# Optimization experiments

Hardware: AMD Instinct MI355X
Metric: run time of the kernel (lower is better)

Reference implementation:

```python
import jax, jax.numpy as jnp
import numpy as np

DIM = 768
HEADS = 12
HEAD_DIM = DIM // HEADS
SCALE = HEAD_DIM ** -0.5


def setup_inputs() -> dict:
    key = jax.random.key(0)
    k1, k2, k3, k4 = jax.random.split(key, 4)
    x = jax.random.normal(k1, (1, 4096, DIM), dtype=jnp.float32)
    # qkv: Linear(dim, 3*dim), bias=False
    W_qkv = jax.random.normal(k2, (DIM, 3 * DIM), dtype=jnp.float32) * (DIM ** -0.5)
    # proj: Linear(dim, dim) with bias
    W_proj = jax.random.normal(k3, (DIM, DIM), dtype=jnp.float32) * (DIM ** -0.5)
    b_proj = jax.random.normal(k4, (DIM,), dtype=jnp.float32) * 0.01
    return {"x": x, "W_qkv": W_qkv, "W_proj": W_proj, "b_proj": b_proj}


def reference(x, W_qkv, W_proj, b_proj):
    b, n, d = x.shape
    qkv = x @ W_qkv                                  # [b, n, 3d]
    q, k, v = jnp.split(qkv, 3, axis=-1)             # each [b, n, d]
    # split heads: [b, n, (h hd)] -> [b, h, n, hd]
    def heads(t):
        return t.reshape(b, n, HEADS, HEAD_DIM).transpose(0, 2, 1, 3)
    q, k, v = heads(q) * SCALE, heads(k), heads(v)
    sim = jnp.einsum('bhid,bhjd->bhij', q, k)        # [b, h, n, n] -- full score matrix
    attn = jax.nn.softmax(sim, axis=-1)
    out = jnp.einsum('bhij,bhjd->bhid', attn, v)     # [b, h, n, hd]
    out = out.transpose(0, 2, 1, 3).reshape(b, n, d)  # merge heads
    return out @ W_proj + b_proj
```

## Files before the change

### kernel.cpp

```cpp
#include <hip/hip_runtime.h>
#include <math.h>

#define TOKENS 4096
#define DMODEL 768
#define NHEADS 12
#define HDIM   64
#define QKV_N  2304
#define ATTN_SCALE 0.125f
#define QSCALE_LOG2E (0.125f * 1.44269504088896340736f)

typedef __attribute__((ext_vector_type(8))) short bf16x8;
typedef __attribute__((ext_vector_type(4))) float floatx4;

__device__ __forceinline__ ushort f2bf(float f) {
    union { float f; unsigned u; } cv; cv.f = f;
    unsigned u = cv.u;
    u += 0x7fffu + ((u >> 16) & 1u);
    return (ushort)(u >> 16);
}

__device__ __forceinline__ unsigned pack_bf16_rne(float a, float b) {
    union { float f; unsigned u; } ca, cb; ca.f = a; cb.f = b;
    unsigned ua = ca.u + 0x7fffu + ((ca.u >> 16) & 1u);
    unsigned ub = cb.u + 0x7fffu + ((cb.u >> 16) & 1u);
    return __builtin_amdgcn_perm(ub, ua, 0x07060302);
}

__device__ __forceinline__ void gl2lds16(const ushort* g, ushort* l) {
    __builtin_amdgcn_global_load_lds(
        (const __attribute__((address_space(1))) void*)g,
        (__attribute__((address_space(3))) void*)l, 16, 0, 0);
}

__device__ __forceinline__ bf16x8 frag(const ushort* ls, int row, int chunk) {
    return *(const bf16x8*)(ls + row * 64 + ((chunk ^ (row & 7)) * 8));
}

__global__ __launch_bounds__(256) void cvt_bf16_kernel(
    const float* __restrict__ in, ushort* __restrict__ out, int n4)
{
    const int i = blockIdx.x * 256 + threadIdx.x;
    if (i < n4) {
        const float4 v = ((const float4*)in)[i];
        ushort4 h;
        h.x = f2bf(v.x); h.y = f2bf(v.y); h.z = f2bf(v.z); h.w = f2bf(v.w);
        ((ushort4*)out)[i] = h;
    }
}

__global__ __launch_bounds__(256) void transpose_cvt_kernel(
    const float* __restrict__ in, ushort* __restrict__ out, int R, int C)
{
    __shared__ ushort tile[32][33];
    const int tx  = threadIdx.x & 31;
    const int ty8 = threadIdx.x >> 5;
    const int c0 = blockIdx.x * 32;
    const int r0 = blockIdx.y * 32;
    #pragma unroll
    for (int p = 0; p < 4; ++p) {
        const int r = ty8 + p * 8;
        tile[r][tx] = f2bf(in[(size_t)(r0 + r) * C + c0 + tx]);
    }
    __syncthreads();
    #pragma unroll
    for (int p = 0; p < 4; ++p) {
        const int c = ty8 + p * 8;
        out[(size_t)(c0 + c) * R + r0 + tx] = tile[tx][c];
    }
}

template<int NT>
__device__ __forceinline__ void gemm_body_async(
    const ushort* __restrict__ A, const ushort* __restrict__ Bt, int K,
    int m0, int n0, floatx4 acc[4][NT], ushort* ls)
{
    ushort* lsA = ls;
    ushort* lsB = ls + 8192;

    const int tid  = threadIdx.x;
    const int lane = tid & 63;
    const int wave = tid >> 6;
    const int wm = wave >> 1, wn = wave & 1;
    const int quad = lane >> 4, l16 = lane & 15;

    const int lrow = lane >> 3;
    const int csw  = ((lane & 7) ^ lrow) * 8;

    const ushort* gA = A  + (size_t)(m0 + wave * 32 + lrow) * K + csw;
    const ushort* gB = Bt + (size_t)(n0 + wave * NT * 8 + lrow) * K + csw;
    ushort* lA = lsA + (wave * 32) * 64;
    ushort* lB = lsB + (wave * NT * 8) * 64;

    for (int k0 = 0; k0 < K; k0 += 64) {
        __syncthreads();
        #pragma unroll
        for (int p = 0; p < 4; ++p)
            gl2lds16(gA + (size_t)p * 8 * K + k0, lA + p * 8 * 64);
        #pragma unroll
        for (int p = 0; p < NT; ++p)
            gl2lds16(gB + (size_t)p * 8 * K + k0, lB + p * 8 * 64);
        __syncthreads();

        #pragma unroll
        for (int ks = 0; ks < 2; ++ks) {
            bf16x8 af[4], bfr[NT];
            #pragma unroll
            for (int mt = 0; mt < 4; ++mt)
                af[mt] = frag(lsA, wm * 64 + mt * 16 + l16, ks * 4 + quad);
            #pragma unroll
            for (int nt = 0; nt < NT; ++nt)
                bfr[nt] = frag(lsB, wn * NT * 16 + nt * 16 + l16, ks * 4 + quad);
            #pragma unroll
            for (int mt = 0; mt < 4; ++mt)
                #pragma unroll
                for (int nt = 0; nt < NT; ++nt)
                    acc[mt][nt] = __builtin_amdgcn_mfma_f32_16x16x32_bf16(
                        af[mt], bfr[nt], acc[mt][nt], 0, 0, 0);
        }
    }
}

__global__ __launch_bounds__(256) void gemm_qkv_mfma(
    const ushort* __restrict__ Xb, const ushort* __restrict__ Wt,
    ushort* __restrict__ Qb, ushort* __restrict__ Kb, ushort* __restrict__ Vt)
{
    __shared__ __align__(16) ushort ls[16384];
    const int m0 = blockIdx.y * 128;
    const int n0 = blockIdx.x * 128;

    floatx4 acc[4][4] = {};
    gemm_body_async<4>(Xb, Wt, DMODEL, m0, n0, acc, ls);

    const int tid  = threadIdx.x;
    const int lane = tid & 63;
    const int wave = tid >> 6;
    const int wm = wave >> 1, wn = wave & 1;
    const int quad = lane >> 4, l16 = lane & 15;

    if (n0 < 2 * DMODEL) {
        const float scale = (n0 < DMODEL) ? QSCALE_LOG2E : 1.0f;
        ushort* outp = (n0 < DMODEL) ? Qb : Kb;
        const int colg = (n0 < DMODEL) ? n0 : n0 - DMODEL;
        #pragma unroll
        for (int p = 0; p < 2; ++p) {
            __syncthreads();
            if (wm == p) {
                #pragma unroll
                for (int mt = 0; mt < 4; ++mt)
                    #pragma unroll
                    for (int nt = 0; nt < 4; ++nt) {
                        const int row = mt * 16 + quad * 4;
                        const int col = wn * 64 + nt * 16 + l16;
                        #pragma unroll
                        for (int r = 0; r < 4; ++r)
                            ls[(row + r) * 136 + col] = f2bf(acc[mt][nt][r] * scale);
                    }
            }
            __syncthreads();
            #pragma unroll
            for (int p2 = 0; p2 < 4; ++p2) {
                const int row = (tid >> 4) + p2 * 16;
                const int c8  = (tid & 15) * 8;
                *(uint4*)(outp + (size_t)(m0 + p * 64 + row) * DMODEL + colg + c8) =
                    *(const uint4*)(ls + row * 136 + c8);
            }
        }
    } else {
        const int hd0 = n0 - 2 * DMODEL;
        #pragma unroll
        for (int p = 0; p < 2; ++p) {
            __syncthreads();
            if (wn == p) {
                #pragma unroll
                for (int mt = 0; mt < 4; ++mt)
                    #pragma unroll
                    for (int nt = 0; nt < 4; ++nt) {
                        const int hd  = nt * 16 + l16;
                        const int tok = wm * 64 + mt * 16 + quad * 4;
                        #pragma unroll
                        for (int r = 0; r < 4; ++r)
                            ls[hd * 136 + tok + r] = f2bf(acc[mt][nt][r]);
                    }
            }
            __syncthreads();
            #pragma unroll
            for (int p2 = 0; p2 < 4; ++p2) {
                const int row = (tid >> 4) + p2 * 16;
                const int c8  = (tid & 15) * 8;
                *(uint4*)(Vt + (size_t)(hd0 + p * 64 + row) * TOKENS + m0 + c8) =
                    *(const uint4*)(ls + row * 136 + c8);
            }
        }
    }
}

__global__ __launch_bounds__(256) void gemm_proj_mfma(
    const ushort* __restrict__ Ab, const ushort* __restrict__ Wt,
    const float* __restrict__ bias, float* __restrict__ out)
{
    __shared__ __align__(16) ushort ls[12288];
    const int m0 = blockIdx.y * 128;
    const int n0 = blockIdx.x * 64;

    floatx4 acc[4][2] = {};
    gemm_body_async<2>(Ab, Wt, DMODEL, m0, n0, acc, ls);

    const int lane = threadIdx.x & 63;
    const int wave = threadIdx.x >> 6;
    const int wm = wave >> 1, wn = wave & 1;
    const int quad = lane >> 4, l16 = lane & 15;
    const int row0 = m0 + wm * 64 + quad * 4;
    const int col0 = n0 + wn * 32;

    #pragma unroll
    for (int nt = 0; nt < 2; ++nt) {
        const int col = col0 + nt * 16 + l16;
        const float bv = bias[col];
        #pragma unroll
        for (int mt = 0; mt < 4; ++mt)
            #pragma unroll
            for (int r = 0; r < 4; ++r)
                out[(size_t)(row0 + mt * 16 + r) * DMODEL + col] =
                    acc[mt][nt][r] + bv;
    }
}

__global__ __launch_bounds__(256) void attn_mfma_kernel(
    const ushort* __restrict__ Qb, const ushort* __restrict__ Kb,
    const ushort* __restrict__ Vt, ushort* __restrict__ attn_out)
{
    __shared__ __align__(16) ushort lds[20480];

    const int tid  = threadIdx.x;
    const int wave = tid >> 6;
    const int lane = tid & 63;
    const int quad = lane >> 4;
    const int l16  = lane & 15;
    const int sw   = (l16 & 7);
    const int h    = blockIdx.y;
    const int i0   = blockIdx.x * 64;

    const ushort* qbase = Qb + (size_t)(i0 + wave * 16 + l16) * DMODEL + h * HDIM;
    const bf16x8 qf0 = *(const bf16x8*)(qbase + quad * 8);
    const bf16x8 qf1 = *(const bf16x8*)(qbase + 32 + quad * 8);

    bf16x8 ones;
    #pragma unroll
    for (int i = 0; i < 8; ++i) ones[i] = (short)0x3F80;

    floatx4 O[4] = {{0.f,0.f,0.f,0.f},{0.f,0.f,0.f,0.f},{0.f,0.f,0.f,0.f},{0.f,0.f,0.f,0.f}};
    floatx4 Ol = {0.f, 0.f, 0.f, 0.f};

    ushort* pw = lds + 16384 + wave * 1024 + l16 * 64;

    const int lrow = lane >> 3;
    const int csw  = ((lane & 7) ^ lrow) * 8;
    const ushort* gK = Kb + (size_t)(wave * 16 + lrow) * DMODEL + h * HDIM + csw;
    const ushort* gV = Vt + (size_t)(h * HDIM + wave * 16 + lrow) * TOKENS + csw;

    #pragma unroll
    for (int p = 0; p < 2; ++p) {
        gl2lds16(gK + (size_t)p * 8 * DMODEL, lds + (wave * 16 + p * 8) * 64);
        gl2lds16(gV + (size_t)p * 8 * TOKENS, lds + 8192 + (wave * 16 + p * 8) * 64);
    }

    for (int j0 = 0; j0 < TOKENS; j0 += 64) {
        const int cur = (j0 >> 6) & 1;
        ushort* Ks = lds + cur * 4096;
        ushort* Vs = lds + 8192 + cur * 4096;
        ushort* Kn = lds + (1 - cur) * 4096;
        ushort* Vn = lds + 8192 + (1 - cur) * 4096;

        __syncthreads();

        if (j0 + 64 < TOKENS) {
            #pragma unroll
            for (int p = 0; p < 2; ++p) {
                gl2lds16(gK + (size_t)(j0 + 64) * DMODEL + (size_t)p * 8 * DMODEL,
                         Kn + (wave * 16 + p * 8) * 64);
                gl2lds16(gV + (size_t)(j0 + 64) + (size_t)p * 8 * TOKENS,
                         Vn + (wave * 16 + p * 8) * 64);
            }
        }

        floatx4 Sv[4];
        #pragma unroll
        for (int jt = 0; jt < 4; ++jt) {
            const bf16x8 k0 = frag(Ks, jt * 16 + l16, quad);
            const bf16x8 k1 = frag(Ks, jt * 16 + l16, 4 + quad);
            floatx4 s = {0.f, 0.f, 0.f, 0.f};
            s = __builtin_amdgcn_mfma_f32_16x16x32_bf16(k0, qf0, s, 0, 0, 0);
            s = __builtin_amdgcn_mfma_f32_16x16x32_bf16(k1, qf1, s, 0, 0, 0);
            Sv[jt] = s;
        }

        #pragma unroll
        for (int jt = 0; jt < 4; ++jt) {
            const float p0 = __builtin_amdgcn_exp2f(Sv[jt][0]);
            const float p1 = __builtin_amdgcn_exp2f(Sv[jt][1]);
            const float p2 = __builtin_amdgcn_exp2f(Sv[jt][2]);
            const float p3 = __builtin_amdgcn_exp2f(Sv[jt][3]);
            uint2 val;
            val.x = pack_bf16_rne(p0, p1);
            val.y = pack_bf16_rne(p2, p3);
            const int chunk = jt * 2 + (quad >> 1);
            *(uint2*)(pw + ((chunk ^ sw) * 8) + (quad & 1) * 4) = val;
        }

        const bf16x8 pf0 = *(const bf16x8*)(pw + ((quad ^ sw) * 8));
        const bf16x8 pf1 = *(const bf16x8*)(pw + (((4 + quad) ^ sw) * 8));

        Ol = __builtin_amdgcn_mfma_f32_16x16x32_bf16(pf0, ones, Ol, 0, 0, 0);
        Ol = __builtin_amdgcn_mfma_f32_16x16x32_bf16(pf1, ones, Ol, 0, 0, 0);

        #pragma unroll
        for (int nt = 0; nt < 4; ++nt) {
            const bf16x8 v0 = frag(Vs, nt * 16 + l16, quad);
            const bf16x8 v1 = frag(Vs, nt * 16 + l16, 4 + quad);
            O[nt] = __builtin_amdgcn_mfma_f32_16x16x32_bf16(pf0, v0, O[nt], 0, 0, 0);
            O[nt] = __builtin_amdgcn_mfma_f32_16x16x32_bf16(pf1, v1, O[nt], 0, 0, 0);
        }
    }

    float linv[4];
    #pragma unroll
    for (int r = 0; r < 4; ++r) linv[r] = __builtin_amdgcn_rcpf(Ol[r]);

    const int orow0 = i0 + wave * 16 + quad * 4;
    #pragma unroll
    for (int nt = 0; nt < 4; ++nt) {
        const int d = h * HDIM + nt * 16 + l16;
        #pragma unroll
        for (int r = 0; r < 4; ++r)
            attn_out[(size_t)(orow0 + r) * DMODEL + d] = f2bf(O[nt][r] * linv[r]);
    }
}

extern "C" void kernel_launch(void* const* d_in, const int* in_sizes, int n_in,
                              void* d_out, int out_size, void* d_ws, size_t ws_size,
                              hipStream_t stream)
{
    const float* x     = (const float*)d_in[0];
    const float* Wqkv  = (const float*)d_in[1];
    const float* Wproj = (const float*)d_in[2];
    const float* bproj = (const float*)d_in[3];
    float* out = (float*)d_out;

    ushort* Xb     = (ushort*)d_ws;
    ushort* WqkvT  = Xb    + (size_t)TOKENS * DMODEL;
    ushort* WprojT = WqkvT + (size_t)QKV_N * DMODEL;
    ushort* Qb     = WprojT + (size_t)DMODEL * DMODEL;
    ushort* Kb     = Qb    + (size_t)TOKENS * DMODEL;
    ushort* Vt     = Kb    + (size_t)TOKENS * DMODEL;
    ushort* attn   = Vt    + (size_t)TOKENS * DMODEL;

    cvt_bf16_kernel<<<dim3(TOKENS * DMODEL / 4 / 256), 256, 0, stream>>>(
        x, Xb, TOKENS * DMODEL / 4);
    transpose_cvt_kernel<<<dim3(QKV_N / 32, DMODEL / 32), 256, 0, stream>>>(
        Wqkv, WqkvT, DMODEL, QKV_N);
    transpose_cvt_kernel<<<dim3(DMODEL / 32, DMODEL / 32), 256, 0, stream>>>(
        Wproj, WprojT, DMODEL, DMODEL);

    gemm_qkv_mfma<<<dim3(QKV_N / 128, TOKENS / 128), 256, 0, stream>>>(
        Xb, WqkvT, Qb, Kb, Vt);

    attn_mfma_kernel<<<dim3(TOKENS / 64, NHEADS), 256, 0, stream>>>(
        Qb, Kb, Vt, attn);

    gemm_proj_mfma<<<dim3(DMODEL / 64, TOKENS / 128), 256, 0, stream>>>(
        attn, WprojT, bproj, out);
}
```

Before: 213.6 us.

## Keep softmax P fragments in registers and permute V reads to match layout

Removes the LDS round-trip for the probability tile. The S accumulator layout is fed directly as the A operand of the PV MFMA, and V fragments are gathered from LDS with a matching permuted k-ordering using two 8-byte reads. The manual round-to-nearest bf16 packing is replaced with the hardware v_cvt_pk_bf16_f32 instruction, and the LDS allocation shrinks. In exchange, V loads become twice as many narrower LDS reads, which may raise bank conflicts.

```diff
diff --git a/kernel.cpp b/kernel.cpp
--- a/kernel.cpp
+++ b/kernel.cpp
@@ -19,11 +19,10 @@
     return (ushort)(u >> 16);
 }
 
-__device__ __forceinline__ unsigned pack_bf16_rne(float a, float b) {
-    union { float f; unsigned u; } ca, cb; ca.f = a; cb.f = b;
-    unsigned ua = ca.u + 0x7fffu + ((ca.u >> 16) & 1u);
-    unsigned ub = cb.u + 0x7fffu + ((cb.u >> 16) & 1u);
-    return __builtin_amdgcn_perm(ub, ua, 0x07060302);
+__device__ __forceinline__ unsigned cvt_pk_bf16(float a, float b) {
+    unsigned r;
+    asm("v_cvt_pk_bf16_f32 %0, %1, %2" : "=v"(r) : "v"(a), "v"(b));
+    return r;
 }
 
 __device__ __forceinline__ void gl2lds16(const ushort* g, ushort* l) {
@@ -229,14 +228,13 @@
     const ushort* __restrict__ Qb, const ushort* __restrict__ Kb,
     const ushort* __restrict__ Vt, ushort* __restrict__ attn_out)
 {
-    __shared__ __align__(16) ushort lds[20480];
+    __shared__ __align__(16) ushort lds[16384];
 
     const int tid  = threadIdx.x;
     const int wave = tid >> 6;
     const int lane = tid & 63;
     const int quad = lane >> 4;
     const int l16  = lane & 15;
-    const int sw   = (l16 & 7);
     const int h    = blockIdx.y;
     const int i0   = blockIdx.x * 64;
 
@@ -250,13 +248,14 @@
 
     floatx4 O[4] = {{0.f,0.f,0.f,0.f},{0.f,0.f,0.f,0.f},{0.f,0.f,0.f,0.f},{0.f,0.f,0.f,0.f}};
     floatx4 Ol = {0.f, 0.f, 0.f, 0.f};
-
-    ushort* pw = lds + 16384 + wave * 1024 + l16 * 64;
 
     const int lrow = lane >> 3;
     const int csw  = ((lane & 7) ^ lrow) * 8;
     const ushort* gK = Kb + (size_t)(wave * 16 + lrow) * DMODEL + h * HDIM + csw;
     const ushort* gV = Vt + (size_t)(h * HDIM + wave * 16 + lrow) * TOKENS + csw;
+
+    const int vhalf = (quad & 1) * 4;
+    const int cb    = quad >> 1;
 
     #pragma unroll
     for (int p = 0; p < 2; ++p) {
@@ -294,31 +293,36 @@
             Sv[jt] = s;
         }
 
+        union { bf16x8 v; unsigned u[4]; } pf0u, pf1u;
         #pragma unroll
         for (int jt = 0; jt < 4; ++jt) {
             const float p0 = __builtin_amdgcn_exp2f(Sv[jt][0]);
             const float p1 = __builtin_amdgcn_exp2f(Sv[jt][1]);
             const float p2 = __builtin_amdgcn_exp2f(Sv[jt][2]);
             const float p3 = __builtin_amdgcn_exp2f(Sv[jt][3]);
-            uint2 val;
-            val.x = pack_bf16_rne(p0, p1);
-            val.y = pack_bf16_rne(p2, p3);
-            const int chunk = jt * 2 + (quad >> 1);
-            *(uint2*)(pw + ((chunk ^ sw) * 8) + (quad & 1) * 4) = val;
-        }
-
-        const bf16x8 pf0 = *(const bf16x8*)(pw + ((quad ^ sw) * 8));
-        const bf16x8 pf1 = *(const bf16x8*)(pw + (((4 + quad) ^ sw) * 8));
+            const unsigned w0 = cvt_pk_bf16(p0, p1);
+            const unsigned w1 = cvt_pk_bf16(p2, p3);
+            if (jt < 2) { pf0u.u[jt * 2] = w0;       pf0u.u[jt * 2 + 1] = w1; }
+            else        { pf1u.u[(jt - 2) * 2] = w0; pf1u.u[(jt - 2) * 2 + 1] = w1; }
+        }
+        const bf16x8 pf0 = pf0u.v;
+        const bf16x8 pf1 = pf1u.v;
 
         Ol = __builtin_amdgcn_mfma_f32_16x16x32_bf16(pf0, ones, Ol, 0, 0, 0);
         Ol = __builtin_amdgcn_mfma_f32_16x16x32_bf16(pf1, ones, Ol, 0, 0, 0);
 
         #pragma unroll
         for (int nt = 0; nt < 4; ++nt) {
-            const bf16x8 v0 = frag(Vs, nt * 16 + l16, quad);
-            const bf16x8 v1 = frag(Vs, nt * 16 + l16, 4 + quad);
-            O[nt] = __builtin_amdgcn_mfma_f32_16x16x32_bf16(pf0, v0, O[nt], 0, 0, 0);
-            O[nt] = __builtin_amdgcn_mfma_f32_16x16x32_bf16(pf1, v1, O[nt], 0, 0, 0);
+            const int r = nt * 16 + l16;
+            const ushort* vrow = Vs + r * 64 + vhalf;
+            const int x = (r & 7);
+            union { bf16x8 v; uint2 u[2]; } v0u, v1u;
+            v0u.u[0] = *(const uint2*)(vrow + ((cb       ^ x) * 8));
+            v0u.u[1] = *(const uint2*)(vrow + (((cb + 2) ^ x) * 8));
+            v1u.u[0] = *(const uint2*)(vrow + (((cb + 4) ^ x) * 8));
+            v1u.u[1] = *(const uint2*)(vrow + (((cb + 6) ^ x) * 8));
+            O[nt] = __builtin_amdgcn_mfma_f32_16x16x32_bf16(pf0, v0u.v, O[nt], 0, 0, 0);
+            O[nt] = __builtin_amdgcn_mfma_f32_16x16x32_bf16(pf1, v1u.v, O[nt], 0, 0, 0);
         }
     }
 
```

Measured after the change: 211.6 us. About the same (-0.9%).
